# Kernel tuning notes

Measured on AMD Instinct MI355X. Metric: run time of the kernel, lower is better.

Reference implementation:

```python
import jax, jax.numpy as jnp
import numpy as np

N_NODES = 50000
N_EDGES = 800000
DIM = 128
N_GRAPHS = 512
LEVELS = [2, 2, 2]  # GCN layers per hierarchy level
N_LAYERS = sum(LEVELS)
EPS = 1e-5


def setup_inputs() -> dict:
    key = jax.random.key(0)
    ks = jax.random.split(key, 8)
    x = jax.random.normal(ks[0], (N_NODES, DIM), dtype=jnp.float32)
    edge_index = jax.random.randint(ks[1], (2, N_EDGES), 0, N_NODES, dtype=jnp.int64)
    batch = jnp.sort(jax.random.randint(ks[2], (N_NODES,), 0, N_GRAPHS, dtype=jnp.int64))
    # stacked per-layer GCN params (all layers are DIM->DIM since input_dim==hidden_dim)
    s = 1.0 / np.sqrt(DIM)
    W = jax.random.uniform(ks[3], (N_LAYERS, DIM, DIM), minval=-s, maxval=s, dtype=jnp.float32)
    b = jnp.zeros((N_LAYERS, DIM), dtype=jnp.float32)
    gamma = jnp.ones((N_LAYERS, DIM), dtype=jnp.float32)
    beta = jnp.zeros((N_LAYERS, DIM), dtype=jnp.float32)
    sf = 1.0 / np.sqrt(DIM * len(LEVELS))
    Wf = jax.random.uniform(ks[4], (DIM * len(LEVELS), DIM), minval=-sf, maxval=sf, dtype=jnp.float32)
    bf = jnp.zeros((DIM,), dtype=jnp.float32)
    return {"x": x, "edge_index": edge_index, "batch": batch,
            "W": W, "b": b, "gamma": gamma, "beta": beta, "Wf": Wf, "bf": bf}


def reference(x, edge_index, batch, W, b, gamma, beta, Wf, bf):
    N = x.shape[0]
    # GCNConv: add self-loops, symmetric normalization deg^-1/2 A_hat deg^-1/2
    loop = jnp.arange(N, dtype=edge_index.dtype)
    src = jnp.concatenate([edge_index[0], loop])
    dst = jnp.concatenate([edge_index[1], loop])
    deg = jax.ops.segment_sum(jnp.ones_like(dst, dtype=x.dtype), dst, num_segments=N)
    dinv = jnp.where(deg > 0, jax.lax.rsqrt(deg), 0.0)
    norm = dinv[src] * dinv[dst]  # (E+N,)

    def gcn(h, Wl, bl):
        h = h @ Wl                                   # (N, DIM)
        msg = h[src] * norm[:, None]                 # gather + scale, (E+N, DIM)
        return jax.ops.segment_sum(msg, dst, num_segments=N) + bl

    def batchnorm_relu(h, g, be):
        mu = jnp.mean(h, axis=0)
        var = jnp.mean(jnp.square(h - mu), axis=0)   # biased var (training-mode BN)
        return jax.nn.relu(g * (h - mu) * jax.lax.rsqrt(var + EPS) + be)

    counts = jax.ops.segment_sum(jnp.ones((N,), x.dtype), batch, num_segments=N_GRAPHS)
    counts = jnp.maximum(counts, 1.0)[:, None]

    reps = []
    h = x
    li = 0
    for num_layers in LEVELS:
        for _ in range(num_layers):
            h = batchnorm_relu(gcn(h, W[li], b[li]), gamma[li], beta[li])
            li += 1
        reps.append(jax.ops.segment_sum(h, batch, num_segments=N_GRAPHS) / counts)
    fused = jnp.concatenate(reps, axis=1)            # (G, 3*DIM)
    return jax.nn.relu(fused @ Wf + bf)              # dropout is identity at inference
```

## Files before the change

### kernel.cpp

```cpp
#include <hip/hip_runtime.h>
#include <hip/hip_fp16.h>


#define DIM 128
#define NGRAPH 512
#define EPSV 1e-5f


__global__ __launch_bounds__(256) void k_count(const int* __restrict__ ei, int* __restrict__ cnt, int E) {
  int e = blockIdx.x * 256 + threadIdx.x;
  if (e < E) atomicAdd(&cnt[ei[E + e]], 1);
}

__global__ __launch_bounds__(512) void k_blocksum(const int* __restrict__ cnt, int* __restrict__ partial, int N) {
  __shared__ int sd[512];
  int idx = blockIdx.x * 512 + threadIdx.x;
  int v = (idx < N) ? cnt[idx] : 0;
  sd[threadIdx.x] = v;
  __syncthreads();
  for (int ofs = 256; ofs > 0; ofs >>= 1) {
    if (threadIdx.x < ofs) sd[threadIdx.x] += sd[threadIdx.x + ofs];
    __syncthreads();
  }
  if (threadIdx.x == 0) partial[blockIdx.x] = sd[0];
}

__global__ __launch_bounds__(128) void k_scanpartials(int* __restrict__ partial, int nb) {
  __shared__ int sp[128];
  int t = threadIdx.x;
  int v = (t < nb) ? partial[t] : 0;
  sp[t] = v;
  __syncthreads();
  for (int ofs = 1; ofs < 128; ofs <<= 1) {
    int a = (t >= ofs) ? sp[t - ofs] : 0;
    __syncthreads();
    sp[t] += a;
    __syncthreads();
  }
  if (t < nb) partial[t] = sp[t] - v;
}

__global__ __launch_bounds__(512) void k_scan_write(const int* __restrict__ cnt, const int* __restrict__ partial,
                                                    int* __restrict__ rowptr, float* __restrict__ dinv, int N) {
  __shared__ int sd[512];
  int tid = threadIdx.x;
  int idx = blockIdx.x * 512 + tid;
  int v = (idx < N) ? cnt[idx] : 0;
  sd[tid] = v;
  __syncthreads();
  for (int ofs = 1; ofs < 512; ofs <<= 1) {
    int a = (tid >= ofs) ? sd[tid - ofs] : 0;
    __syncthreads();
    sd[tid] += a;
    __syncthreads();
  }
  if (idx < N) {
    int excl = partial[blockIdx.x] + sd[tid] - v;
    rowptr[idx] = excl;
    dinv[idx] = rsqrtf((float)(v + 1));
    if (idx == N - 1) rowptr[N] = excl + v;
  }
}

__global__ __launch_bounds__(256) void k_fill(const int* __restrict__ ei, const int* __restrict__ rowptr,
                                              int* __restrict__ cursor, int* __restrict__ cols, int E) {
  int e = blockIdx.x * 256 + threadIdx.x;
  if (e >= E) return;
  int s = ei[e];
  int d = ei[E + e];
  int pos = rowptr[d] + atomicAdd(&cursor[d], 1);
  cols[pos] = s;
}

__global__ __launch_bounds__(256) void k_gstart(const int* __restrict__ batch, int* __restrict__ start, int N) {
  int i = blockIdx.x * 256 + threadIdx.x;
  if (i >= N) return;
  int bi = batch[i];
  int prev = (i == 0) ? -1 : batch[i - 1];
  for (int g = prev + 1; g <= bi; ++g) start[g] = i;
  if (i == N - 1) {
    for (int g = bi + 1; g <= NGRAPH; ++g) start[g] = N;
  }
}

__global__ __launch_bounds__(512) void k_invcnt(const int* __restrict__ start, float* __restrict__ invcnt) {
  int g = threadIdx.x;
  if (g < NGRAPH) {
    int c = start[g + 1] - start[g];
    invcnt[g] = 1.0f / (float)max(c, 1);
  }
}


__device__ inline void fma4(float4& ar, float a, const float4& wv) {
  ar.x = fmaf(a, wv.x, ar.x);
  ar.y = fmaf(a, wv.y, ar.y);
  ar.z = fmaf(a, wv.z, ar.z);
  ar.w = fmaf(a, wv.w, ar.w);
}

__global__ __launch_bounds__(256) void k_gemm(const float* __restrict__ A, const float* __restrict__ Wl,
                                              const float* __restrict__ scsh,
                                              const float* __restrict__ dinv,
                                              unsigned int* __restrict__ T, float* __restrict__ stats, int N) {
  __shared__ float sH[32][DIM];
  int tid = threadIdx.x;
  size_t pstride = (size_t)(N + 1) * 16;
  if (blockIdx.x == 0) {
    stats[tid] = 0.f;
    if (tid < 64) {
      int p = tid >> 4, sl = tid & 15;
      T[(size_t)p * pstride + (size_t)N * 16 + sl] = 0u;
    }
  }
  int row0 = blockIdx.x * 32;
#pragma unroll
  for (int i = 0; i < 4; ++i) {
    int fi = tid + i * 256;
    int r = fi >> 5, c4 = fi & 31;
    int row = row0 + r;
    float4 v = make_float4(0.f, 0.f, 0.f, 0.f);
    if (row < N) v = ((const float4*)(A + (size_t)row * DIM))[c4];
    if (scsh) {
      float4 sc = ((const float4*)scsh)[c4];
      float4 sh = ((const float4*)(scsh + DIM))[c4];
      v.x = fmaxf(fmaf(v.x, sc.x, sh.x), 0.f);
      v.y = fmaxf(fmaf(v.y, sc.y, sh.y), 0.f);
      v.z = fmaxf(fmaf(v.z, sc.z, sh.z), 0.f);
      v.w = fmaxf(fmaf(v.w, sc.w, sh.w), 0.f);
    }
    ((float4*)&sH[r][0])[c4] = v;
  }
  __syncthreads();
  int ct = tid & 31, rt = tid >> 5;
  const float4* Wv = (const float4*)Wl;
  float4 acc[4];
#pragma unroll
  for (int r = 0; r < 4; ++r) acc[r] = make_float4(0.f, 0.f, 0.f, 0.f);
  for (int k4 = 0; k4 < 32; ++k4) {
    float4 wv0 = Wv[(4 * k4 + 0) * 32 + ct];
    float4 wv1 = Wv[(4 * k4 + 1) * 32 + ct];
    float4 wv2 = Wv[(4 * k4 + 2) * 32 + ct];
    float4 wv3 = Wv[(4 * k4 + 3) * 32 + ct];
#pragma unroll
    for (int r = 0; r < 4; ++r) {
      float4 av = *(const float4*)&sH[rt + 8 * r][4 * k4];
      fma4(acc[r], av.x, wv0);
      fma4(acc[r], av.y, wv1);
      fma4(acc[r], av.z, wv2);
      fma4(acc[r], av.w, wv3);
    }
  }
  int panel = ct >> 3;
  int psl = (ct & 7) * 2;
  unsigned int* Tp = T + (size_t)panel * pstride;
#pragma unroll
  for (int r = 0; r < 4; ++r) {
    int row = row0 + rt + 8 * r;
    if (row < N) {
      float dr = dinv[row];
      __half2 h0 = __floats2half2_rn(acc[r].x * dr, acc[r].y * dr);
      __half2 h1 = __floats2half2_rn(acc[r].z * dr, acc[r].w * dr);
      uint2 packed = make_uint2(*(unsigned int*)&h0, *(unsigned int*)&h1);
      *(uint2*)(Tp + (size_t)row * 16 + psl) = packed;
    }
  }
}

__global__ __launch_bounds__(256) void k_agg(const unsigned int* __restrict__ T, const int* __restrict__ rowptr,
                                             const int* __restrict__ cols, const float* __restrict__ dinv,
                                             const float* __restrict__ bias, float* __restrict__ hout,
                                             float* __restrict__ stats, int N) {
  int phase = blockIdx.x & 3;
  int chunk = blockIdx.x >> 2;
  int nchunks = gridDim.x >> 2;
  int tid = threadIdx.x;
  int wid = __builtin_amdgcn_readfirstlane(tid >> 6);
  int lane = tid & 63;
  int sub = lane >> 4;
  int slot = lane & 15;
  const unsigned int* __restrict__ Tp = T + (size_t)phase * (N + 1) * 16;
  float bx = bias[phase * 32 + 2 * slot];
  float by = bias[phase * 32 + 2 * slot + 1];
  int gwave = chunk * 4 + wid;
  int nwaves = nchunks * 4;
  float sum0 = 0.f, sum1 = 0.f, sq0 = 0.f, sq1 = 0.f;
  for (int i = gwave; i < N; i += nwaves) {
    float ax = 0.f, ay = 0.f;
    if (sub == 0) {
      unsigned int u0 = Tp[(size_t)i * 16 + slot];
      float2 t0 = __half22float2(*(__half2*)&u0);
      ax = t0.x;
      ay = t0.y;
    }
    int beg = rowptr[i], end = rowptr[i + 1];
    for (int e0 = beg; e0 < end; e0 += 32) {
      int ss[8];
#pragma unroll
      for (int k = 0; k < 8; ++k) {
        int eidx = e0 + 4 * k + sub;
        int cv = cols[eidx];
        ss[k] = (eidx < end) ? cv : N;
      }
      unsigned int uu[8];
#pragma unroll
      for (int k = 0; k < 8; ++k) uu[k] = Tp[(size_t)ss[k] * 16 + slot];
#pragma unroll
      for (int k = 0; k < 8; ++k) {
        float2 t = __half22float2(*(__half2*)&uu[k]);
        ax += t.x;
        ay += t.y;
      }
    }
    ax += __shfl_xor(ax, 16);
    ay += __shfl_xor(ay, 16);
    ax += __shfl_xor(ax, 32);
    ay += __shfl_xor(ay, 32);
    if (sub == 0) {
      float di = dinv[i];
      ax = fmaf(di, ax, bx);
      ay = fmaf(di, ay, by);
      ((float2*)(hout + (size_t)i * DIM + phase * 32))[slot] = make_float2(ax, ay);
      sum0 += ax;
      sum1 += ay;
      sq0 = fmaf(ax, ax, sq0);
      sq1 = fmaf(ay, ay, sq1);
    }
  }
  __shared__ float red[4][16][4];
  if (sub == 0) {
    red[wid][slot][0] = sum0;
    red[wid][slot][1] = sum1;
    red[wid][slot][2] = sq0;
    red[wid][slot][3] = sq1;
  }
  __syncthreads();
  if (tid < 16) {
    int sl = tid;
    float a0 = red[0][sl][0] + red[1][sl][0] + red[2][sl][0] + red[3][sl][0];
    float a1 = red[0][sl][1] + red[1][sl][1] + red[2][sl][1] + red[3][sl][1];
    float q0 = red[0][sl][2] + red[1][sl][2] + red[2][sl][2] + red[3][sl][2];
    float q1 = red[0][sl][3] + red[1][sl][3] + red[2][sl][3] + red[3][sl][3];
    int c0 = phase * 32 + 2 * sl;
    atomicAdd(&stats[c0], a0);
    atomicAdd(&stats[c0 + 1], a1);
    atomicAdd(&stats[DIM + c0], q0);
    atomicAdd(&stats[DIM + c0 + 1], q1);
  }
}

__global__ __launch_bounds__(128) void k_bnstat(float* __restrict__ stats, const float* __restrict__ gamma,
                                                const float* __restrict__ beta, int N) {
  int c = threadIdx.x;
  float invN = 1.f / (float)N;
  float mu = stats[c] * invN;
  float var = stats[DIM + c] * invN - mu * mu;
  float rstd = rsqrtf(var + EPSV);
  float sc = gamma[c] * rstd;
  stats[2 * DIM + c] = sc;
  stats[3 * DIM + c] = beta[c] - mu * sc;
}

__global__ __launch_bounds__(512) void k_pool(const float* __restrict__ h, const int* __restrict__ start,
                                              const float* __restrict__ invcnt, const float* __restrict__ scsh,
                                              float* __restrict__ pooled, int level) {
  int g = blockIdx.x;
  int s = start[g], e = start[g + 1];
  int c = threadIdx.x & 127;
  int stripe = threadIdx.x >> 7;
  float sc = scsh[c], sh = scsh[DIM + c];
  float acc = 0.f;
  for (int r = s + stripe; r < e; r += 4) acc += fmaxf(fmaf(h[(size_t)r * DIM + c], sc, sh), 0.f);
  __shared__ float red[4][DIM];
  red[stripe][c] = acc;
  __syncthreads();
  if (threadIdx.x < DIM) {
    float v = (red[0][c] + red[1][c] + red[2][c] + red[3][c]) * invcnt[g];
    pooled[(size_t)g * (3 * DIM) + level * DIM + c] = v;
  }
}

__global__ __launch_bounds__(512) void k_final(const float* __restrict__ pooled, const float* __restrict__ Wf,
                                               const float* __restrict__ bf, float* __restrict__ out) {
  int t = blockIdx.x * 512 + threadIdx.x;
  if (t >= NGRAPH * DIM) return;
  int j = t & (DIM - 1);
  int i = t >> 7;
  const float* prow = pooled + (size_t)i * (3 * DIM);
  float acc = bf[j];
  for (int k = 0; k < 3 * DIM; ++k) acc = fmaf(prow[k], Wf[(size_t)k * DIM + j], acc);
  out[t] = fmaxf(acc, 0.f);
}


extern "C" void kernel_launch(void* const* d_in, const int* in_sizes, int n_in,
                              void* d_out, int out_size, void* d_ws, size_t ws_size,
                              hipStream_t stream) {
  const float* x = (const float*)d_in[0];
  const int* ei = (const int*)d_in[1];
  const int* batch = (const int*)d_in[2];
  const float* W = (const float*)d_in[3];
  const float* b = (const float*)d_in[4];
  const float* gamma = (const float*)d_in[5];
  const float* beta = (const float*)d_in[6];
  const float* Wf = (const float*)d_in[7];
  const float* bf = (const float*)d_in[8];
  float* out = (float*)d_out;

  const int N = in_sizes[0] / DIM;
  const int E = in_sizes[1] / 2;

  char* base = (char*)d_ws;
  size_t off = 0;
  auto alloc = [&](size_t bytes) -> char* {
    char* p = base + off;
    off += (bytes + 255) & ~(size_t)255;
    return p;
  };
  float* h          = (float*)alloc((size_t)N * DIM * 4);
  unsigned int* T   = (unsigned int*)alloc((size_t)(N + 1) * DIM * 2);
  int* cnt          = (int*)alloc((size_t)N * 4);
  int* cursor       = (int*)alloc((size_t)N * 4);
  int* rowptr       = (int*)alloc((size_t)(N + 1) * 4);
  int* partial      = (int*)alloc(256 * 4);
  float* dinv       = (float*)alloc((size_t)N * 4);
  int* cols         = (int*)alloc((size_t)(E + 32) * 4);
  float* stats      = (float*)alloc(4 * DIM * 4);
  int* start        = (int*)alloc((NGRAPH + 1) * 4);
  float* invcnt     = (float*)alloc(NGRAPH * 4);
  float* pooled     = (float*)alloc((size_t)NGRAPH * 3 * DIM * 4);
  (void)ws_size;

  (void)hipMemsetAsync(cnt, 0, (size_t)N * 4, stream);
  (void)hipMemsetAsync(cursor, 0, (size_t)N * 4, stream);

  int nbScan = (N + 511) / 512;
  k_count<<<(E + 255) / 256, 256, 0, stream>>>(ei, cnt, E);
  k_blocksum<<<nbScan, 512, 0, stream>>>(cnt, partial, N);
  k_scanpartials<<<1, 128, 0, stream>>>(partial, nbScan);
  k_scan_write<<<nbScan, 512, 0, stream>>>(cnt, partial, rowptr, dinv, N);
  k_fill<<<(E + 255) / 256, 256, 0, stream>>>(ei, rowptr, cursor, cols, E);
  k_gstart<<<(N + 255) / 256, 256, 0, stream>>>(batch, start, N);
  k_invcnt<<<1, 512, 0, stream>>>(start, invcnt);

  int gemmGrid = (N + 31) / 32;
  for (int l = 0; l < 6; ++l) {
    const float* hin = (l == 0) ? x : h;
    const float* scsh = (l == 0) ? nullptr : stats + 2 * DIM;
    k_gemm<<<gemmGrid, 256, 0, stream>>>(hin, W + (size_t)l * DIM * DIM, scsh, dinv, T, stats, N);
    k_agg<<<2048, 256, 0, stream>>>(T, rowptr, cols, dinv, b + (size_t)l * DIM, h, stats, N);
    k_bnstat<<<1, 128, 0, stream>>>(stats, gamma + (size_t)l * DIM, beta + (size_t)l * DIM, N);
    if (l & 1) k_pool<<<NGRAPH, 512, 0, stream>>>(h, start, invcnt, stats + 2 * DIM, pooled, l >> 1);
  }
  k_final<<<(NGRAPH * DIM + 511) / 512, 512, 0, stream>>>(pooled, Wf, bf, out);
}
```

Measured before the change: 812.3 us.

## Store activations in fp16, compress edge indices to uint16, widen GEMM row tile

The aggregation output h is now written as packed half2 instead of fp32. The next layer's GEMM and the pooling kernel read and convert these fp16 values. CSR column indices are stored as 16-bit unsigned shorts, which only works while N stays below 65536, and the GEMM tile grows from 32 to 64 rows per block. The aim is to halve the activation and index memory traffic per layer and to reuse W loads across more rows, at the cost of fp16 rounding of pre-BN activations and more registers per thread in the GEMM.

```diff
diff --git a/kernel.cpp b/kernel.cpp
--- a/kernel.cpp
+++ b/kernel.cpp
@@ -63,13 +63,13 @@
 }
 
 __global__ __launch_bounds__(256) void k_fill(const int* __restrict__ ei, const int* __restrict__ rowptr,
-                                              int* __restrict__ cursor, int* __restrict__ cols, int E) {
+                                              int* __restrict__ cursor, unsigned short* __restrict__ cols, int E) {
   int e = blockIdx.x * 256 + threadIdx.x;
   if (e >= E) return;
   int s = ei[e];
   int d = ei[E + e];
   int pos = rowptr[d] + atomicAdd(&cursor[d], 1);
-  cols[pos] = s;
+  cols[pos] = (unsigned short)s;
 }
 
 __global__ __launch_bounds__(256) void k_gstart(const int* __restrict__ batch, int* __restrict__ start, int N) {
@@ -99,11 +99,13 @@
   ar.w = fmaf(a, wv.w, ar.w);
 }
 
-__global__ __launch_bounds__(256) void k_gemm(const float* __restrict__ A, const float* __restrict__ Wl,
+__global__ __launch_bounds__(256) void k_gemm(const float* __restrict__ A32,
+                                              const unsigned int* __restrict__ A16,
+                                              const float* __restrict__ Wl,
                                               const float* __restrict__ scsh,
                                               const float* __restrict__ dinv,
                                               unsigned int* __restrict__ T, float* __restrict__ stats, int N) {
-  __shared__ float sH[32][DIM];
+  __shared__ float sH[64][DIM];
   int tid = threadIdx.x;
   size_t pstride = (size_t)(N + 1) * 16;
   if (blockIdx.x == 0) {
@@ -113,37 +115,43 @@
       T[(size_t)p * pstride + (size_t)N * 16 + sl] = 0u;
     }
   }
-  int row0 = blockIdx.x * 32;
-#pragma unroll
-  for (int i = 0; i < 4; ++i) {
+  int row0 = blockIdx.x * 64;
+#pragma unroll
+  for (int i = 0; i < 8; ++i) {
     int fi = tid + i * 256;
     int r = fi >> 5, c4 = fi & 31;
     int row = row0 + r;
     float4 v = make_float4(0.f, 0.f, 0.f, 0.f);
-    if (row < N) v = ((const float4*)(A + (size_t)row * DIM))[c4];
     if (scsh) {
-      float4 sc = ((const float4*)scsh)[c4];
-      float4 sh = ((const float4*)(scsh + DIM))[c4];
-      v.x = fmaxf(fmaf(v.x, sc.x, sh.x), 0.f);
-      v.y = fmaxf(fmaf(v.y, sc.y, sh.y), 0.f);
-      v.z = fmaxf(fmaf(v.z, sc.z, sh.z), 0.f);
-      v.w = fmaxf(fmaf(v.w, sc.w, sh.w), 0.f);
+      if (row < N) {
+        uint2 u = ((const uint2*)(A16 + (size_t)row * 64))[c4];
+        float2 lo = __half22float2(*(__half2*)&u.x);
+        float2 hi = __half22float2(*(__half2*)&u.y);
+        float4 sc = ((const float4*)scsh)[c4];
+        float4 sh = ((const float4*)(scsh + DIM))[c4];
+        v.x = fmaxf(fmaf(lo.x, sc.x, sh.x), 0.f);
+        v.y = fmaxf(fmaf(lo.y, sc.y, sh.y), 0.f);
+        v.z = fmaxf(fmaf(hi.x, sc.z, sh.z), 0.f);
+        v.w = fmaxf(fmaf(hi.y, sc.w, sh.w), 0.f);
+      }
+    } else {
+      if (row < N) v = ((const float4*)(A32 + (size_t)row * DIM))[c4];
     }
     ((float4*)&sH[r][0])[c4] = v;
   }
   __syncthreads();
   int ct = tid & 31, rt = tid >> 5;
   const float4* Wv = (const float4*)Wl;
-  float4 acc[4];
-#pragma unroll
-  for (int r = 0; r < 4; ++r) acc[r] = make_float4(0.f, 0.f, 0.f, 0.f);
+  float4 acc[8];
+#pragma unroll
+  for (int r = 0; r < 8; ++r) acc[r] = make_float4(0.f, 0.f, 0.f, 0.f);
   for (int k4 = 0; k4 < 32; ++k4) {
     float4 wv0 = Wv[(4 * k4 + 0) * 32 + ct];
     float4 wv1 = Wv[(4 * k4 + 1) * 32 + ct];
     float4 wv2 = Wv[(4 * k4 + 2) * 32 + ct];
     float4 wv3 = Wv[(4 * k4 + 3) * 32 + ct];
 #pragma unroll
-    for (int r = 0; r < 4; ++r) {
+    for (int r = 0; r < 8; ++r) {
       float4 av = *(const float4*)&sH[rt + 8 * r][4 * k4];
       fma4(acc[r], av.x, wv0);
       fma4(acc[r], av.y, wv1);
@@ -155,7 +163,7 @@
   int psl = (ct & 7) * 2;
   unsigned int* Tp = T + (size_t)panel * pstride;
 #pragma unroll
-  for (int r = 0; r < 4; ++r) {
+  for (int r = 0; r < 8; ++r) {
     int row = row0 + rt + 8 * r;
     if (row < N) {
       float dr = dinv[row];
@@ -168,8 +176,8 @@
 }
 
 __global__ __launch_bounds__(256) void k_agg(const unsigned int* __restrict__ T, const int* __restrict__ rowptr,
-                                             const int* __restrict__ cols, const float* __restrict__ dinv,
-                                             const float* __restrict__ bias, float* __restrict__ hout,
+                                             const unsigned short* __restrict__ cols, const float* __restrict__ dinv,
+                                             const float* __restrict__ bias, unsigned int* __restrict__ hout,
                                              float* __restrict__ stats, int N) {
   int phase = blockIdx.x & 3;
   int chunk = blockIdx.x >> 2;
@@ -199,7 +207,7 @@
 #pragma unroll
       for (int k = 0; k < 8; ++k) {
         int eidx = e0 + 4 * k + sub;
-        int cv = cols[eidx];
+        int cv = (int)cols[eidx];
         ss[k] = (eidx < end) ? cv : N;
       }
       unsigned int uu[8];
@@ -220,7 +228,8 @@
       float di = dinv[i];
       ax = fmaf(di, ax, bx);
       ay = fmaf(di, ay, by);
-      ((float2*)(hout + (size_t)i * DIM + phase * 32))[slot] = make_float2(ax, ay);
+      __half2 hp = __floats2half2_rn(ax, ay);
+      hout[(size_t)i * 64 + phase * 16 + slot] = *(unsigned int*)&hp;
       sum0 += ax;
       sum1 += ay;
       sq0 = fmaf(ax, ax, sq0);
@@ -261,22 +270,38 @@
   stats[3 * DIM + c] = beta[c] - mu * sc;
 }
 
-__global__ __launch_bounds__(512) void k_pool(const float* __restrict__ h, const int* __restrict__ start,
+__global__ __launch_bounds__(512) void k_pool(const unsigned int* __restrict__ h16, const int* __restrict__ start,
                                               const float* __restrict__ invcnt, const float* __restrict__ scsh,
                                               float* __restrict__ pooled, int level) {
   int g = blockIdx.x;
   int s = start[g], e = start[g + 1];
-  int c = threadIdx.x & 127;
-  int stripe = threadIdx.x >> 7;
-  float sc = scsh[c], sh = scsh[DIM + c];
-  float acc = 0.f;
-  for (int r = s + stripe; r < e; r += 4) acc += fmaxf(fmaf(h[(size_t)r * DIM + c], sc, sh), 0.f);
-  __shared__ float red[4][DIM];
-  red[stripe][c] = acc;
-  __syncthreads();
-  if (threadIdx.x < DIM) {
-    float v = (red[0][c] + red[1][c] + red[2][c] + red[3][c]) * invcnt[g];
-    pooled[(size_t)g * (3 * DIM) + level * DIM + c] = v;
+  int slot = threadIdx.x & 63;
+  int stripe = threadIdx.x >> 6;
+  float scx = scsh[2 * slot], scy = scsh[2 * slot + 1];
+  float shx = scsh[DIM + 2 * slot], shy = scsh[DIM + 2 * slot + 1];
+  float ax = 0.f, ay = 0.f;
+  for (int r = s + stripe; r < e; r += 8) {
+    unsigned int u = h16[(size_t)r * 64 + slot];
+    float2 t = __half22float2(*(__half2*)&u);
+    ax += fmaxf(fmaf(t.x, scx, shx), 0.f);
+    ay += fmaxf(fmaf(t.y, scy, shy), 0.f);
+  }
+  __shared__ float red[8][64][2];
+  red[stripe][slot][0] = ax;
+  red[stripe][slot][1] = ay;
+  __syncthreads();
+  if (threadIdx.x < 64) {
+    int sl = threadIdx.x;
+    float vx = 0.f, vy = 0.f;
+#pragma unroll
+    for (int st = 0; st < 8; ++st) {
+      vx += red[st][sl][0];
+      vy += red[st][sl][1];
+    }
+    float ic = invcnt[g];
+    float* dst = pooled + (size_t)g * (3 * DIM) + level * DIM + 2 * sl;
+    dst[0] = vx * ic;
+    dst[1] = vy * ic;
   }
 }
 
@@ -317,14 +342,14 @@
     off += (bytes + 255) & ~(size_t)255;
     return p;
   };
-  float* h          = (float*)alloc((size_t)N * DIM * 4);
+  unsigned int* h16 = (unsigned int*)alloc((size_t)N * DIM * 2);
   unsigned int* T   = (unsigned int*)alloc((size_t)(N + 1) * DIM * 2);
   int* cnt          = (int*)alloc((size_t)N * 4);
   int* cursor       = (int*)alloc((size_t)N * 4);
   int* rowptr       = (int*)alloc((size_t)(N + 1) * 4);
   int* partial      = (int*)alloc(256 * 4);
   float* dinv       = (float*)alloc((size_t)N * 4);
-  int* cols         = (int*)alloc((size_t)(E + 32) * 4);
+  unsigned short* cols = (unsigned short*)alloc((size_t)(E + 32) * 2);
   float* stats      = (float*)alloc(4 * DIM * 4);
   int* start        = (int*)alloc((NGRAPH + 1) * 4);
   float* invcnt     = (float*)alloc(NGRAPH * 4);
@@ -343,14 +368,14 @@
   k_gstart<<<(N + 255) / 256, 256, 0, stream>>>(batch, start, N);
   k_invcnt<<<1, 512, 0, stream>>>(start, invcnt);
 
-  int gemmGrid = (N + 31) / 32;
+  int gemmGrid = (N + 63) / 64;
   for (int l = 0; l < 6; ++l) {
-    const float* hin = (l == 0) ? x : h;
     const float* scsh = (l == 0) ? nullptr : stats + 2 * DIM;
-    k_gemm<<<gemmGrid, 256, 0, stream>>>(hin, W + (size_t)l * DIM * DIM, scsh, dinv, T, stats, N);
-    k_agg<<<2048, 256, 0, stream>>>(T, rowptr, cols, dinv, b + (size_t)l * DIM, h, stats, N);
+    k_gemm<<<gemmGrid, 256, 0, stream>>>((l == 0) ? x : nullptr, (l == 0) ? nullptr : h16,
+                                         W + (size_t)l * DIM * DIM, scsh, dinv, T, stats, N);
+    k_agg<<<2048, 256, 0, stream>>>(T, rowptr, cols, dinv, b + (size_t)l * DIM, h16, stats, N);
     k_bnstat<<<1, 128, 0, stream>>>(stats, gamma + (size_t)l * DIM, beta + (size_t)l * DIM, N);
-    if (l & 1) k_pool<<<NGRAPH, 512, 0, stream>>>(h, start, invcnt, stats + 2 * DIM, pooled, l >> 1);
+    if (l & 1) k_pool<<<NGRAPH, 512, 0, stream>>>(h16, start, invcnt, stats + 2 * DIM, pooled, l >> 1);
   }
   k_final<<<(NGRAPH * DIM + 511) / 512, 512, 0, stream>>>(pooled, Wf, bf, out);
 }
```

Result: faster. 779.4 us (-4.1%).
